# Kernel tuning notes

Hardware: AMD Instinct MI355X
Metric: run time of the kernel (lower is better)

## Reference

```python
import jax, jax.numpy as jnp
import numpy as np

B, T, HID = 2, 2048, 2048
H, KVH, DK, DV = 32, 8, 128, 128
NORM_EPS = 1e-5
L2_EPS = 1e-6


def setup_inputs() -> dict:
    key = jax.random.key(0)
    ks = jax.random.split(key, 11)
    s = 0.02  # xavier-ish scale
    # dt_bias init as in the module: dt ~ logU(1e-3, 1e-1); inv_dt = dt + log(-expm1(-dt))
    u = jax.random.uniform(ks[9], (H,))
    dt = jnp.exp(u * (np.log(0.1) - np.log(0.001)) + np.log(0.001))
    dt = jnp.clip(dt, 1e-4, None)
    dt_bias = dt + jnp.log(-jnp.expm1(-dt))
    A = jax.random.uniform(ks[10], (H,), minval=1e-3, maxval=16.0)
    return {
        "hidden_states": jax.random.normal(ks[0], (B, T, HID), jnp.float32),
        "Wq": jax.random.normal(ks[1], (HID, H * DK), jnp.float32) * s,
        "Wk": jax.random.normal(ks[2], (HID, KVH * DK), jnp.float32) * s,
        "Wv": jax.random.normal(ks[3], (HID, KVH * DV), jnp.float32) * s,
        "Wb": jax.random.normal(ks[4], (HID, H), jnp.float32) * s,
        "Wa": jax.random.normal(ks[5], (HID, H), jnp.float32) * s,
        "Wg": jax.random.normal(ks[6], (HID, H * DV), jnp.float32) * s,
        "Wo": jax.random.normal(ks[7], (H * DV, HID), jnp.float32) * s,
        "A_log": jnp.log(A),
        "dt_bias": dt_bias,
        "o_norm_w": jnp.ones((DV,), jnp.float32),
    }


def _l2norm(x):
    return x * jax.lax.rsqrt(jnp.sum(x * x, axis=-1, keepdims=True) + L2_EPS)


def _gated_delta_rule(q, k, v, g, beta):
    """q,k,v: [B,T,H,D]; g,beta: [B,T,H]. Returns o: [B,T,H,DV].
    Recurrence (per head):
      S_t = exp(g_t) * S_{t-1}
      u_t = beta_t * (v_t - k_t @ S_t)
      S_t = S_t + k_t^T u_t
      o_t = (q_t / sqrt(DK)) @ S_t
    """
    scale = DK ** -0.5
    q = q * scale

    def step(S, xs):
        q_t, k_t, v_t, g_t, b_t = xs  # [B,H,DK]/[B,H,DV]/[B,H]
        S = S * jnp.exp(g_t)[..., None, None]                      # [B,H,DK,DV]
        v_adj = (v_t - jnp.einsum('bhk,bhkv->bhv', k_t, S)) * b_t[..., None]
        S = S + k_t[..., :, None] * v_adj[..., None, :]
        o_t = jnp.einsum('bhk,bhkv->bhv', q_t, S)
        return S, o_t

    S0 = jnp.zeros((B, H, DK, DV), q.dtype)
    xs = tuple(jnp.moveaxis(a, 1, 0) for a in (q, k, v, g, beta))
    _, o = jax.lax.scan(step, S0, xs)
    return jnp.moveaxis(o, 0, 1)


def reference(hidden_states, Wq, Wk, Wv, Wb, Wa, Wg, Wo, A_log, dt_bias, o_norm_w):
    h = hidden_states
    q = (h @ Wq).reshape(B, T, H, DK)
    k = (h @ Wk).reshape(B, T, KVH, DK)
    v = (h @ Wv).reshape(B, T, KVH, DV)
    q = _l2norm(q)
    k = _l2norm(k)
    beta = jax.nn.sigmoid(h @ Wb) * 2.0                             # [B,T,H]
    g = -jnp.exp(A_log) * jax.nn.softplus(h @ Wa + dt_bias)         # [B,T,H]
    grp = H // KVH
    k = jnp.repeat(k, grp, axis=2)                                  # GQA expand
    v = jnp.repeat(v, grp, axis=2)
    o = _gated_delta_rule(q, k, v, g, beta)                         # [B,T,H,DV]
    # FusedRMSNormSwishGate: rmsnorm(o)*w * swish(gate)
    gate = (h @ Wg).reshape(B, T, H, DV)
    o = o * jax.lax.rsqrt(jnp.mean(o * o, axis=-1, keepdims=True) + NORM_EPS) * o_norm_w
    o = o * gate * jax.nn.sigmoid(gate)
    return o.reshape(B, T, H * DV) @ Wo
```

## Files before the change

### kernel.cpp

```cpp
#include <hip/hip_runtime.h>
#include <stdint.h>


#define B_ 2
#define T_ 2048
#define HID_ 2048
#define H_ 32
#define KVH_ 8
#define M_ (B_*T_)
#define NQKV 6144
#define NGBA 4224
#define NALL (NQKV + NGBA)
#define OFS_K 4096
#define OFS_V 5120
#define OFS_B2 4096
#define OFS_A2 4128

typedef unsigned short u16;
typedef unsigned int u32;
typedef __attribute__((ext_vector_type(2))) float f32x2;
typedef __attribute__((ext_vector_type(4))) float f32x4;
typedef __attribute__((ext_vector_type(2))) u32 u32x2;
typedef __attribute__((ext_vector_type(8))) __bf16 bf16x8;

__device__ __forceinline__ u16 f2b(float f) {
  u32 u = __builtin_bit_cast(u32, f);
  u32 r = (u + 0x7FFFu + ((u >> 16) & 1u)) >> 16;
  return (u16)r;
}
__device__ __forceinline__ float b2f(u16 x) {
  u32 u = ((u32)x) << 16;
  return __builtin_bit_cast(float, u);
}

__global__ __launch_bounds__(256) void fill_k(float* __restrict__ p, int n, float v) {
  int i = blockIdx.x * 256 + threadIdx.x;
  if (i < n) p[i] = v;
}

__global__ __launch_bounds__(256) void cast_bf16_k(const float* __restrict__ in,
                                                   u16* __restrict__ out, int n4) {
  int i = blockIdx.x * 256 + threadIdx.x;
  if (i >= n4) return;
  f32x4 v = ((const f32x4*)in)[i];
  u32x2 p;
  p.x = (u32)f2b(v.x) | ((u32)f2b(v.y) << 16);
  p.y = (u32)f2b(v.z) | ((u32)f2b(v.w) << 16);
  ((u32x2*)out)[i] = p;
}

__global__ __launch_bounds__(256) void transpose_cast_k(const float* __restrict__ in,
                                                        u16* __restrict__ out, int R, int C) {
  __shared__ float tile[32][33];
  int bc = blockIdx.x * 32, br = blockIdx.y * 32;
  int tx = threadIdx.x & 31, ty = threadIdx.x >> 5;
#pragma unroll
  for (int i = ty; i < 32; i += 8) tile[i][tx] = in[(size_t)(br + i) * C + bc + tx];
  __syncthreads();
#pragma unroll
  for (int i = ty; i < 32; i += 8) out[(size_t)(bc + i) * R + br + tx] = f2b(tile[tx][i]);
}

template <int OUT_BF16>
__global__ __launch_bounds__(256) void gemm_nt_k(const u16* __restrict__ A, const u16* __restrict__ Bt,
                                                 void* __restrict__ Cv, int M, int N, int K) {
  __shared__ u16 As[128 * 32];
  __shared__ u16 Bs[128 * 32];
  int tid = threadIdx.x;
  int lane = tid & 63, wid = tid >> 6;
  int wm = wid >> 1, wn = wid & 1;
  int bm = blockIdx.y << 7, bn = blockIdx.x << 7;
  int r16 = lane & 15, kp = (lane >> 4) << 3;
  f32x4 acc[4][4] = {};
  for (int k0 = 0; k0 < K; k0 += 32) {
    __syncthreads();
#pragma unroll
    for (int half = 0; half < 2; ++half) {
      int c = tid + (half << 8);
      int row = c >> 2, kc = (c & 3) << 3;
      const u16* g = A + (size_t)(bm + row) * K + k0 + kc;
      __builtin_amdgcn_global_load_lds((const __attribute__((address_space(1))) void*)g,
          (__attribute__((address_space(3))) void*)((char*)As + (size_t)((wid << 6) + (half << 8)) * 16),
          16, 0, 0);
    }
#pragma unroll
    for (int half = 0; half < 2; ++half) {
      int c = tid + (half << 8);
      int row = c >> 2, kc = (c & 3) << 3;
      const u16* g = Bt + (size_t)(bn + row) * K + k0 + kc;
      __builtin_amdgcn_global_load_lds((const __attribute__((address_space(1))) void*)g,
          (__attribute__((address_space(3))) void*)((char*)Bs + (size_t)((wid << 6) + (half << 8)) * 16),
          16, 0, 0);
    }
    asm volatile("s_waitcnt vmcnt(0)" ::: "memory");
    __syncthreads();
    bf16x8 af[4], bfv[4];
#pragma unroll
    for (int i = 0; i < 4; ++i) af[i] = *(const bf16x8*)&As[(size_t)((wm << 6) + (i << 4) + r16) * 32 + kp];
#pragma unroll
    for (int j = 0; j < 4; ++j) bfv[j] = *(const bf16x8*)&Bs[(size_t)((wn << 6) + (j << 4) + r16) * 32 + kp];
#pragma unroll
    for (int i = 0; i < 4; ++i)
#pragma unroll
      for (int j = 0; j < 4; ++j)
        acc[i][j] = __builtin_amdgcn_mfma_f32_16x16x32_bf16(af[i], bfv[j], acc[i][j], 0, 0, 0);
  }
  int rg = (lane >> 4) << 2;
#pragma unroll
  for (int i = 0; i < 4; ++i)
#pragma unroll
    for (int j = 0; j < 4; ++j)
#pragma unroll
      for (int r = 0; r < 4; ++r) {
        int row = bm + (wm << 6) + (i << 4) + rg + r;
        int col = bn + (wn << 6) + (j << 4) + r16;
        if (OUT_BF16) ((u16*)Cv)[(size_t)row * N + col] = f2b(acc[i][j][r]);
        else          ((float*)Cv)[(size_t)row * N + col] = acc[i][j][r];
      }
}

__global__ __launch_bounds__(256) void ew1_k(const u16* __restrict__ qkv,
                                             float* __restrict__ Qb, float* __restrict__ KVb) {
  const int BTH = B_ * T_ * H_;
  const int BTKV = B_ * T_ * KVH_;
  int row = blockIdx.x * 4 + (threadIdx.x >> 6);
  int lane = threadIdx.x & 63;
  const u16* src; float* dst; int donorm = 1; float extra = 1.0f;
  if (row < BTH) {
    int hh = row & 31; int bt = row >> 5;
    src = qkv + (size_t)bt * NQKV + (hh << 7);
    int b = bt >> 11, t = bt & 2047;
    dst = Qb + ((size_t)(b * H_ + hh) * T_ + t) * 128;
    extra = 0.08838834764831843f;
  } else if (row < BTH + BTKV) {
    int r2 = row - BTH; int kh = r2 & 7; int bt = r2 >> 3;
    src = qkv + (size_t)bt * NQKV + OFS_K + (kh << 7);
    int b = bt >> 11, t = bt & 2047;
    dst = KVb + ((size_t)(b * KVH_ + kh) * T_ + t) * 256;
  } else {
    int r2 = row - BTH - BTKV; int kh = r2 & 7; int bt = r2 >> 3;
    src = qkv + (size_t)bt * NQKV + OFS_V + (kh << 7);
    int b = bt >> 11, t = bt & 2047;
    dst = KVb + ((size_t)(b * KVH_ + kh) * T_ + t) * 256 + 128;
    donorm = 0;
  }
  u32 raw = ((const u32*)src)[lane];
  float x0 = b2f((u16)raw), x1 = b2f((u16)(raw >> 16));
  if (donorm) {
    float ss = x0 * x0 + x1 * x1;
    ss += __shfl_xor(ss, 1);  ss += __shfl_xor(ss, 2);  ss += __shfl_xor(ss, 4);
    ss += __shfl_xor(ss, 8);  ss += __shfl_xor(ss, 16); ss += __shfl_xor(ss, 32);
    float sc = extra / sqrtf(ss + 1e-6f);
    x0 *= sc; x1 *= sc;
  }
  f32x2 o; o.x = x0; o.y = x1;
  ((f32x2*)dst)[lane] = o;
}

__global__ __launch_bounds__(256) void eb_k(const u16* __restrict__ gba,
                                            const float* __restrict__ A_log,
                                            const float* __restrict__ dt_bias,
                                            f32x2* __restrict__ EB) {
  int i = blockIdx.x * 256 + threadIdx.x;
  int hh = i & 31; int bt = i >> 5;
  int t = bt & 2047, b = bt >> 11;
  const u16* rowp = gba + (size_t)bt * NGBA;
  float braw = b2f(rowp[OFS_B2 + hh]);
  float araw = b2f(rowp[OFS_A2 + hh]);
  float beta = 2.0f / (1.0f + expf(-braw));
  float x = araw + dt_bias[hh];
  float sp = (x > 20.0f) ? x : log1pf(expf(x));
  float g = -expf(A_log[hh]) * sp;
  f32x2 e; e.x = expf(g); e.y = beta;
  EB[((size_t)(b * H_ + hh)) * T_ + t] = e;
}

struct StepB { f32x4 k[4]; f32x4 q[4]; f32x2 eb; float v; };

__global__ __launch_bounds__(64) void scan_k(const float* __restrict__ Qb, const float* __restrict__ KVb,
                                             const f32x2* __restrict__ EB, float* __restrict__ O) {
  int idx = blockIdx.x;
  int head = idx & 63, dvg = idx >> 6;
  int b = head >> 5, hh = head & 31;
  int lane = threadIdx.x;
  int dkq = lane & 7, dvl = lane >> 3;
  int dv0 = dvg << 3;
  const f32x4* qp = (const f32x4*)(Qb + ((size_t)(b * H_ + hh) * T_) * 128) + (dkq << 2);
  const f32x4* kp = (const f32x4*)(KVb + ((size_t)(b * KVH_ + (hh >> 2)) * T_) * 256) + (dkq << 2);
  const float* vp = KVb + ((size_t)(b * KVH_ + (hh >> 2)) * T_) * 256 + 128 + dv0 + dvl;
  const f32x2* ep = EB + (size_t)(b * H_ + hh) * T_;
  float* op = O + (size_t)b * T_ * H_ * 128 + hh * 128 + dv0 + dvl;

  f32x4 S[4] = {};
  StepB s[4];
#pragma unroll
  for (int j = 0; j < 4; ++j) {
#pragma unroll
    for (int c = 0; c < 4; ++c) { s[j].k[c] = kp[j * 64 + c]; s[j].q[c] = qp[j * 32 + c]; }
    s[j].v = vp[(size_t)j * 256]; s[j].eb = ep[j];
  }
  for (int t = 0; t < T_; t += 4) {
#pragma unroll
    for (int j = 0; j < 4; ++j) {
      int tt = t + j;
      f32x4 a = s[j].k[0] * S[0] + s[j].k[1] * S[1] + s[j].k[2] * S[2] + s[j].k[3] * S[3];
      float kS = a.x + a.y + a.z + a.w;
      kS += __shfl_xor(kS, 1); kS += __shfl_xor(kS, 2); kS += __shfl_xor(kS, 4);
      float eg = s[j].eb.x, beta = s[j].eb.y;
      float vadj = (s[j].v - eg * kS) * beta;
      S[0] = S[0] * eg + s[j].k[0] * vadj;
      S[1] = S[1] * eg + s[j].k[1] * vadj;
      S[2] = S[2] * eg + s[j].k[2] * vadj;
      S[3] = S[3] * eg + s[j].k[3] * vadj;
      f32x4 ob = s[j].q[0] * S[0] + s[j].q[1] * S[1] + s[j].q[2] * S[2] + s[j].q[3] * S[3];
      float o = ob.x + ob.y + ob.z + ob.w;
      o += __shfl_xor(o, 1); o += __shfl_xor(o, 2); o += __shfl_xor(o, 4);
      if (dkq == 0) op[(size_t)tt * (H_ * 128)] = o;
      int nt = tt + 4; if (nt >= T_) nt = T_ - 1;
#pragma unroll
      for (int c = 0; c < 4; ++c) { s[j].k[c] = kp[(size_t)nt * 64 + c]; s[j].q[c] = qp[(size_t)nt * 32 + c]; }
      s[j].v = vp[(size_t)nt * 256]; s[j].eb = ep[nt];
    }
  }
}

__global__ __launch_bounds__(256) void ew2_k(const float* __restrict__ O, const u16* __restrict__ gba,
                                             const float* __restrict__ w, u16* __restrict__ Xo) {
  int r = blockIdx.x * 4 + (threadIdx.x >> 6);
  int lane = threadIdx.x & 63;
  f32x2 ov = ((const f32x2*)(O + (size_t)r * 128))[lane];
  float ss = ov.x * ov.x + ov.y * ov.y;
  ss += __shfl_xor(ss, 1);  ss += __shfl_xor(ss, 2);  ss += __shfl_xor(ss, 4);
  ss += __shfl_xor(ss, 8);  ss += __shfl_xor(ss, 16); ss += __shfl_xor(ss, 32);
  float rms = 1.0f / sqrtf(ss * (1.0f / 128.0f) + 1e-5f);
  f32x2 wv = ((const f32x2*)w)[lane];
  int hh = r & 31; size_t bt = (size_t)(r >> 5);
  u32 graw = ((const u32*)(gba + bt * NGBA + (hh << 7)))[lane];
  float g0 = b2f((u16)graw), g1 = b2f((u16)(graw >> 16));
  float y0 = ov.x * rms * wv.x * (g0 / (1.0f + expf(-g0)));
  float y1 = ov.y * rms * wv.y * (g1 / (1.0f + expf(-g1)));
  u32 pk = (u32)f2b(y0) | ((u32)f2b(y1) << 16);
  ((u32*)(Xo + bt * 4096 + (hh << 7)))[lane] = pk;
}

extern "C" void kernel_launch(void* const* d_in, const int* in_sizes, int n_in,
                              void* d_out, int out_size, void* d_ws, size_t ws_size,
                              hipStream_t stream) {
  const float* h    = (const float*)d_in[0];
  const float* Wq   = (const float*)d_in[1];
  const float* Wk   = (const float*)d_in[2];
  const float* Wv   = (const float*)d_in[3];
  const float* Wb   = (const float*)d_in[4];
  const float* Wa   = (const float*)d_in[5];
  const float* Wg   = (const float*)d_in[6];
  const float* Wo   = (const float*)d_in[7];
  const float* Alog = (const float*)d_in[8];
  const float* dtb  = (const float*)d_in[9];
  const float* onw  = (const float*)d_in[10];

  constexpr size_t SZ_X     = (size_t)M_ * HID_ * 2;
  constexpr size_t SZ_WALLT = (size_t)NALL * HID_ * 2;
  constexpr size_t SZ_WOT   = (size_t)HID_ * 4096 * 2;
  constexpr size_t SZ_QKV   = (size_t)M_ * NQKV * 2;
  constexpr size_t SZ_GBA   = (size_t)M_ * NGBA * 2;
  constexpr size_t SZ_QB    = (size_t)B_ * H_ * T_ * 128 * 4;
  constexpr size_t SZ_KVB   = (size_t)B_ * KVH_ * T_ * 256 * 4;
  constexpr size_t SZ_EB    = (size_t)B_ * H_ * T_ * 8;
  constexpr size_t SZ_O     = (size_t)M_ * H_ * 128 * 4;
  constexpr size_t SZ_U1    = SZ_QB;
  constexpr size_t SZ_U2    = SZ_O;
  constexpr size_t NEED = SZ_U1 + SZ_WOT + SZ_GBA + SZ_U2 + SZ_KVB + SZ_EB;

  if (ws_size < NEED) {
    fill_k<<<dim3((out_size + 255) / 256), dim3(256), 0, stream>>>((float*)d_out, out_size, 12345.0f);
    return;
  }

  char* base   = (char*)d_ws;
  char* segU1  = base;
  char* segWot = segU1 + SZ_U1;
  char* segGBA = segWot + SZ_WOT;
  char* segU2  = segGBA + SZ_GBA;
  char* segKVB = segU2 + SZ_U2;
  char* segEB  = segKVB + SZ_KVB;

  u16*   X     = (u16*)segU1;
  u16*   Wallt = (u16*)(segU1 + SZ_X);
  u16*   Wot   = (u16*)segWot;
  u16*   qkv   = (u16*)segU2;
  u16*   gba   = (u16*)segGBA;
  float* Qb    = (float*)segU1;
  float* KVb   = (float*)segKVB;
  f32x2* EB    = (f32x2*)segEB;
  float* O     = (float*)segU2;
  u16*   Xo    = (u16*)segU1;

  cast_bf16_k<<<dim3(M_ * HID_ / 4 / 256), dim3(256), 0, stream>>>(h, X, M_ * HID_ / 4);

  transpose_cast_k<<<dim3(4096/32, 2048/32), dim3(256), 0, stream>>>(Wq, Wallt, 2048, 4096);
  transpose_cast_k<<<dim3(1024/32, 2048/32), dim3(256), 0, stream>>>(Wk, Wallt + (size_t)4096 * HID_, 2048, 1024);
  transpose_cast_k<<<dim3(1024/32, 2048/32), dim3(256), 0, stream>>>(Wv, Wallt + (size_t)5120 * HID_, 2048, 1024);
  transpose_cast_k<<<dim3(4096/32, 2048/32), dim3(256), 0, stream>>>(Wg, Wallt + (size_t)6144 * HID_, 2048, 4096);
  transpose_cast_k<<<dim3(32/32,   2048/32), dim3(256), 0, stream>>>(Wb, Wallt + (size_t)10240 * HID_, 2048, 32);
  transpose_cast_k<<<dim3(32/32,   2048/32), dim3(256), 0, stream>>>(Wa, Wallt + (size_t)10272 * HID_, 2048, 32);
  hipMemsetAsync(Wallt + (size_t)10304 * HID_, 0, (size_t)64 * HID_ * 2, stream);
  transpose_cast_k<<<dim3(2048/32, 4096/32), dim3(256), 0, stream>>>(Wo, Wot, 4096, 2048);

  gemm_nt_k<1><<<dim3(NQKV/128, M_/128), dim3(256), 0, stream>>>(X, Wallt, qkv, M_, NQKV, HID_);
  gemm_nt_k<1><<<dim3(NGBA/128, M_/128), dim3(256), 0, stream>>>(X, Wallt + (size_t)NQKV * HID_, gba, M_, NGBA, HID_);

  ew1_k<<<dim3((B_*T_*H_ + 2*B_*T_*KVH_) / 4), dim3(256), 0, stream>>>(qkv, Qb, KVb);
  eb_k<<<dim3(B_*H_*T_ / 256), dim3(256), 0, stream>>>(gba, Alog, dtb, EB);

  scan_k<<<dim3(B_*H_ * 16), dim3(64), 0, stream>>>(Qb, KVb, EB, O);

  ew2_k<<<dim3(B_*T_*H_ / 4), dim3(256), 0, stream>>>(O, gba, onw, Xo);

  gemm_nt_k<0><<<dim3(2048/128, M_/128), dim3(256), 0, stream>>>(Xo, Wot, d_out, M_, 2048, 4096);
}
```

Before: 1.575 ms.

## Fuse next-step k·S reduction with q·S output reduction in scan

Measured after the change: 1.524 ms. -3.2%, faster.

```diff
diff --git a/kernel.cpp b/kernel.cpp
--- a/kernel.cpp
+++ b/kernel.cpp
@@ -175,8 +175,6 @@
   EB[((size_t)(b * H_ + hh)) * T_ + t] = e;
 }
 
-struct StepB { f32x4 k[4]; f32x4 q[4]; f32x2 eb; float v; };
-
 __global__ __launch_bounds__(64) void scan_k(const float* __restrict__ Qb, const float* __restrict__ KVb,
                                              const f32x2* __restrict__ EB, float* __restrict__ O) {
   int idx = blockIdx.x;
@@ -189,37 +187,41 @@
   const f32x4* kp = (const f32x4*)(KVb + ((size_t)(b * KVH_ + (hh >> 2)) * T_) * 256) + (dkq << 2);
   const float* vp = KVb + ((size_t)(b * KVH_ + (hh >> 2)) * T_) * 256 + 128 + dv0 + dvl;
   const f32x2* ep = EB + (size_t)(b * H_ + hh) * T_;
-  float* op = O + (size_t)b * T_ * H_ * 128 + hh * 128 + dv0 + dvl;
+  float* op = O + (size_t)b * T_ * (H_ * 128) + hh * 128 + dv0 + dvl;
 
   f32x4 S[4] = {};
-  StepB s[4];
+  f32x4 kb[4][4], qb[4][4];
+  float vb[4]; f32x2 eb[4];
 #pragma unroll
   for (int j = 0; j < 4; ++j) {
 #pragma unroll
-    for (int c = 0; c < 4; ++c) { s[j].k[c] = kp[j * 64 + c]; s[j].q[c] = qp[j * 32 + c]; }
-    s[j].v = vp[(size_t)j * 256]; s[j].eb = ep[j];
-  }
+    for (int c = 0; c < 4; ++c) { kb[j][c] = kp[j * 64 + c]; qb[j][c] = qp[j * 32 + c]; }
+    vb[j] = vp[(size_t)j * 256]; eb[j] = ep[j];
+  }
+  float kS = 0.0f;
   for (int t = 0; t < T_; t += 4) {
 #pragma unroll
     for (int j = 0; j < 4; ++j) {
       int tt = t + j;
-      f32x4 a = s[j].k[0] * S[0] + s[j].k[1] * S[1] + s[j].k[2] * S[2] + s[j].k[3] * S[3];
-      float kS = a.x + a.y + a.z + a.w;
-      kS += __shfl_xor(kS, 1); kS += __shfl_xor(kS, 2); kS += __shfl_xor(kS, 4);
-      float eg = s[j].eb.x, beta = s[j].eb.y;
-      float vadj = (s[j].v - eg * kS) * beta;
-      S[0] = S[0] * eg + s[j].k[0] * vadj;
-      S[1] = S[1] * eg + s[j].k[1] * vadj;
-      S[2] = S[2] * eg + s[j].k[2] * vadj;
-      S[3] = S[3] * eg + s[j].k[3] * vadj;
-      f32x4 ob = s[j].q[0] * S[0] + s[j].q[1] * S[1] + s[j].q[2] * S[2] + s[j].q[3] * S[3];
-      float o = ob.x + ob.y + ob.z + ob.w;
-      o += __shfl_xor(o, 1); o += __shfl_xor(o, 2); o += __shfl_xor(o, 4);
-      if (dkq == 0) op[(size_t)tt * (H_ * 128)] = o;
-      int nt = tt + 4; if (nt >= T_) nt = T_ - 1;
-#pragma unroll
-      for (int c = 0; c < 4; ++c) { s[j].k[c] = kp[(size_t)nt * 64 + c]; s[j].q[c] = qp[(size_t)nt * 32 + c]; }
-      s[j].v = vp[(size_t)nt * 256]; s[j].eb = ep[nt];
+      float eg = eb[j].x, beta = eb[j].y;
+      float vadj = (vb[j] - eg * kS) * beta;
+#pragma unroll
+      for (int c = 0; c < 4; ++c) S[c] = S[c] * eg + kb[j][c] * vadj;
+      const int jn = (j + 1) & 3;
+      f32x4 p4 = kb[jn][0] * S[0] + kb[jn][1] * S[1] + kb[jn][2] * S[2] + kb[jn][3] * S[3];
+      f32x4 r4 = qb[j][0] * S[0] + qb[j][1] * S[1] + qb[j][2] * S[2] + qb[j][3] * S[3];
+      int nt = tt + 4; if (nt > T_ - 1) nt = T_ - 1;
+#pragma unroll
+      for (int c = 0; c < 4; ++c) { kb[j][c] = kp[(size_t)nt * 64 + c]; qb[j][c] = qp[(size_t)nt * 32 + c]; }
+      vb[j] = vp[(size_t)nt * 256]; eb[j] = ep[nt];
+      float p = (p4.x + p4.y) + (p4.z + p4.w);
+      float r = (r4.x + r4.y) + (r4.z + r4.w);
+      p += __shfl_xor(p, 1);  r += __shfl_xor(r, 1);
+      p += __shfl_xor(p, 2);  r += __shfl_xor(r, 2);
+      p += __shfl_xor(p, 4);  r += __shfl_xor(r, 4);
+      kS = p;
+      if (dkq == 0) op[(size_t)tt * (H_ * 128)] = r;
+      __builtin_amdgcn_sched_barrier(0);
     }
   }
 }
```
